# Performance work log

Measured on AMD Instinct MI355X. Metric: run time of the kernel, lower is better.

The kernel has to match this reference:

```python
import jax, jax.numpy as jnp
import numpy as np

MAX_LEN, BATCH, EMB = 512, 32, 41
HID, UNITS = 800, 20
BOND_LENS = jnp.array([1.329, 1.459, 1.525], jnp.float32)
BOND_ANGLES = jnp.array([2.034, 2.119, 1.937], jnp.float32)
INIT_ABC = jnp.array([[0.0, 0.0, 1.0], [0.0, 1.0, 0.0], [1.0, 0.0, 0.0]], jnp.float32)


def _lstm_dir(x, w_ih, w_hh, b, reverse):
    # x: [T, B, in]; returns hidden states [T, B, H]
    T, B, _ = x.shape
    H = w_hh.shape[1]
    xs = jnp.flip(x, 0) if reverse else x
    xw = jnp.einsum('tbi,gi->tbg', xs, w_ih) + b  # precompute input projection

    def step(carry, xt):
        h, c = carry
        gates = xt + h @ w_hh.T
        i, f, g, o = jnp.split(gates, 4, axis=-1)
        c = jax.nn.sigmoid(f) * c + jax.nn.sigmoid(i) * jnp.tanh(g)
        h = jax.nn.sigmoid(o) * jnp.tanh(c)
        return (h, c), h

    init = (jnp.zeros((B, H), x.dtype), jnp.zeros((B, H), x.dtype))
    _, hs = jax.lax.scan(step, init, xw)
    return jnp.flip(hs, 0) if reverse else hs


def _bilstm_layer(x, w_ih, w_hh, b):
    # w_ih: [2, 4H, in]; w_hh: [2, 4H, H]; b: [2, 4H]
    fwd = _lstm_dir(x, w_ih[0], w_hh[0], b[0], False)
    bwd = _lstm_dir(x, w_ih[1], w_hh[1], b[1], True)
    return jnp.concatenate([fwd, bwd], axis=-1)


def _geometric_unit(coords3, triplet):
    # coords3: [3, B, 3] last three atoms; triplet: [B, 3] torsion angles
    A, Bc, C = coords3[0], coords3[1], coords3[2]
    new = []
    for i in range(3):
        Tang, R, P = BOND_ANGLES[i], BOND_LENS[i], triplet[:, i]
        D2 = jnp.stack([-R * jnp.cos(Tang) * jnp.ones_like(P),
                        R * jnp.cos(P) * jnp.sin(Tang),
                        R * jnp.sin(P) * jnp.sin(Tang)], axis=1)  # [B,3]
        BC = C - Bc
        bc = BC / jnp.linalg.norm(BC, axis=1, keepdims=True)
        AB = Bc - A
        N = jnp.cross(AB, bc)
        n = N / jnp.linalg.norm(N, axis=1, keepdims=True)
        M = jnp.stack([bc, jnp.cross(n, bc), n], axis=2)  # [B,3,3]
        D = jnp.einsum('bij,bj->bi', M, D2) + C
        A, Bc, C = Bc, C, D
        new.append(D)
    return jnp.stack([A, Bc, C]), jnp.stack(new)  # carry, [3,B,3]


def setup_inputs() -> dict:
    key = jax.random.key(0)
    ks = jax.random.split(key, 10)
    k = 1.0 / np.sqrt(HID)
    u = lambda kk, shp, lim: jax.random.uniform(kk, shp, jnp.float32, -lim, lim)
    in0, in1 = EMB + 1, 2 * HID
    return {
        'sequences': jax.random.normal(ks[0], (MAX_LEN, BATCH, EMB), jnp.float32),
        'lengths': jnp.full((BATCH,), MAX_LEN, jnp.int64 if jax.config.jax_enable_x64 else jnp.int32),
        'w_ih0': u(ks[1], (2, 4 * HID, in0), k),
        'w_hh0': u(ks[2], (2, 4 * HID, HID), k),
        'b0': u(ks[3], (2, 4 * HID), k),
        'w_ih1': u(ks[4], (2, 4 * HID, in1), k),
        'w_hh1': u(ks[5], (2, 4 * HID, HID), k),
        'b1': u(ks[6], (2, 4 * HID), k),
        'lin_w': u(ks[7], (UNITS, 2 * HID), 1.0 / np.sqrt(2 * HID)),
        'lin_b': u(ks[8], (UNITS,), 1.0 / np.sqrt(2 * HID)),
        'alphabet': jax.random.uniform(ks[9], (UNITS, 3), jnp.float32, -3.14, 3.14),
    }


def reference(sequences, lengths, w_ih0, w_hh0, b0, w_ih1, w_hh1, b1, lin_w, lin_b, alphabet):
    T, B, _ = sequences.shape
    abs_pos = jnp.broadcast_to(jnp.arange(T, dtype=sequences.dtype)[:, None, None], (T, B, 1))
    x = jnp.concatenate([sequences, abs_pos], axis=2)  # [T, B, EMB+1]
    # 2-layer bidirectional LSTM (all lengths == max_len -> packing is identity)
    h = _bilstm_layer(x, w_ih0, w_hh0, b0)
    h = _bilstm_layer(h, w_ih1, w_hh1, b1)  # [T, B, 2H]
    # linear -> softmax over alphabet, trig angle decode
    soft = jax.nn.softmax(h @ lin_w.T + lin_b, axis=2)  # [T, B, UNITS]
    sine = soft @ jnp.sin(alphabet)   # [T, B, 3]
    cosine = soft @ jnp.cos(alphabet)
    out = jnp.arctan2(sine, cosine)   # torsion angle triplets
    # sequential geometric coordinate recurrence over timesteps 1..T-1
    init = jnp.broadcast_to(INIT_ABC[:, None, :], (3, B, 3))
    _, new_coords = jax.lax.scan(_geometric_unit, init, out[1:])  # [T-1, 3, B, 3]
    pred_coords = jnp.concatenate([init, new_coords.reshape(-1, B, 3)], axis=0)
    return pred_coords  # [3 + 3*(T-1), B, 3]
```

## Files before the change

kernel.cpp:

```cpp
#include <hip/hip_runtime.h>
#include <math.h>

#define T_LEN 512
#define NB    32
#define EMB_  41
#define IN0_  42
#define HID_  800
#define G4_   3200
#define IN1_  1600
#define NU    20
#define NCH   100
#define NREP  8

typedef unsigned short u16;
typedef unsigned int   u32;
typedef unsigned long long u64;
typedef __attribute__((ext_vector_type(8))) short short8;
typedef __attribute__((ext_vector_type(4))) float f32x4;

__device__ __forceinline__ float bf2f(u16 v) {
    union { u32 u; float f; } c; c.u = ((u32)v) << 16; return c.f;
}
__device__ __forceinline__ u16 f2bf(float f) {
    union { float f; u32 u; } c; c.f = f;
    u32 r = (c.u + 0x7fffu + ((c.u >> 16) & 1u)) >> 16;
    return (u16)r;
}
__device__ __forceinline__ short cvt_hl(float v, int hl) {
    u16 hi = f2bf(v);
    return hl ? (short)f2bf(v - bf2f(hi)) : (short)hi;
}
__device__ __forceinline__ f32x4 mfma16(short8 a, short8 b, f32x4 c) {
    return __builtin_amdgcn_mfma_f32_16x16x32_bf16(a, b, c, 0, 0, 0);
}
__device__ __forceinline__ u64 aload(const u64* p) {
    return __hip_atomic_load(p, __ATOMIC_RELAXED, __HIP_MEMORY_SCOPE_AGENT);
}
__device__ __forceinline__ void astore(u64* p, u64 v) {
    __hip_atomic_store(p, v, __ATOMIC_RELAXED, __HIP_MEMORY_SCOPE_AGENT);
}
__device__ __forceinline__ int afload(const int* p) {
    return __hip_atomic_load(p, __ATOMIC_RELAXED, __HIP_MEMORY_SCOPE_AGENT);
}
__device__ __forceinline__ void afstore(int* p, int v) {
    __hip_atomic_store(p, v, __ATOMIC_RELAXED, __HIP_MEMORY_SCOPE_AGENT);
}

__global__ __launch_bounds__(256, 1)
void lstm0_persist(const float* __restrict__ seq, const float* __restrict__ wih0,
                   const float* __restrict__ whh0, const float* __restrict__ bias,
                   u16* __restrict__ h0f, u16* __restrict__ hB, int* __restrict__ flags)
{
    __shared__ __align__(16) float part[2048];
    __shared__ __align__(16) u16 stageB[25600];
    __shared__ __align__(16) float w0l[32*48];
    __shared__ __align__(16) float xsl[32*48];
    __shared__ u16 hpk[NB*8];
    const int tid = threadIdx.x;
    const int d = blockIdx.x / NCH, ch = blockIdx.x % NCH;
    const int w = tid >> 6, l = tid & 63;
    const int p = w & 1, hl = w >> 1;
    int* myflags = flags + d*NCH*16;

    short8 wreg[25];
    {
        const int m = l & 15, g = p*2 + (m>>3), j = ch*8 + (m&7);
        const float* base = whh0 + ((size_t)(d*G4_ + g*HID_ + j))*HID_ + (l>>4)*8;
#pragma unroll
        for (int kc = 0; kc < 25; ++kc) {
            float4 f0 = *(const float4*)(base + kc*32);
            float4 f1 = *(const float4*)(base + kc*32 + 4);
            short8 v;
            v[0]=cvt_hl(f0.x,hl); v[1]=cvt_hl(f0.y,hl); v[2]=cvt_hl(f0.z,hl); v[3]=cvt_hl(f0.w,hl);
            v[4]=cvt_hl(f1.x,hl); v[5]=cvt_hl(f1.y,hl); v[6]=cvt_hl(f1.z,hl); v[7]=cvt_hl(f1.w,hl);
            wreg[kc] = v;
        }
    }
    for (int idx = tid; idx < 32*EMB_; idx += 256) {
        int r = idx / EMB_, k = idx % EMB_;
        int ju_ = r >> 2, g = r & 3;
        w0l[r*48 + k] = wih0[((size_t)(d*G4_ + g*HID_ + ch*8 + ju_))*IN0_ + k];
    }
    const int ju = tid >> 5, b = tid & 31;
    const int j = ch*8 + ju;
    const int nt = b >> 4, n = b & 15;
    float biasr[4], wpos[4];
#pragma unroll
    for (int g = 0; g < 4; ++g) {
        biasr[g] = bias[d*G4_ + g*HID_ + j];
        wpos[g]  = wih0[((size_t)(d*G4_ + g*HID_ + j))*IN0_ + EMB_];
    }
    float creg = 0.f;
    __syncthreads();

    for (int s = 0; s < T_LEN; ++s) {
        const int t = d ? (T_LEN-1-s) : s;
        const u64* hq64 = (const u64*)(hB + (size_t)((s&1)*2 + d)*25600);
        u64*      hnq  = (u64*)(hB + (size_t)(((s&1)^1)*2 + d)*25600);

        for (int idx = tid; idx < 32*EMB_; idx += 256)
            xsl[(idx/EMB_)*48 + idx%EMB_] = seq[(size_t)t*(NB*EMB_) + idx];

        if (s > 0 && tid < NCH)
            while (afload(myflags + tid*16) < s) __builtin_amdgcn_s_sleep(1);
        __syncthreads();

        {
            u64 tmp[25];
#pragma unroll
            for (int q = 0; q < 25; ++q) tmp[q] = aload(hq64 + tid + q*256);
#pragma unroll
            for (int q = 0; q < 25; ++q) ((u64*)stageB)[tid + q*256] = tmp[q];
        }
        __syncthreads();

        f32x4 acc0 = {0.f,0.f,0.f,0.f}, acc1 = {0.f,0.f,0.f,0.f};
#pragma unroll 5
        for (int kc = 0; kc < 25; ++kc) {
            short8 b0 = *(const short8*)(stageB + kc*1024 + l*8);
            short8 b1 = *(const short8*)(stageB + kc*1024 + 512 + l*8);
            acc0 = mfma16(wreg[kc], b0, acc0);
            acc1 = mfma16(wreg[kc], b1, acc1);
        }
        {
            const int mrow = (l>>4)*4, nn = l & 15;
#pragma unroll
            for (int r = 0; r < 4; ++r) {
                part[(((p*2+hl)*2 + 0)*16 + mrow + r)*16 + nn] = acc0[r];
                part[(((p*2+hl)*2 + 1)*16 + mrow + r)*16 + nn] = acc1[r];
            }
        }
        __syncthreads();

        float dot0 = 0.f, dot1 = 0.f, dot2 = 0.f, dot3 = 0.f;
        {
            const float* wr = &w0l[ju*4*48];
            const float* xr = &xsl[b*48];
#pragma unroll
            for (int k4 = 0; k4 < 40; k4 += 4) {
                float4 xk = *(const float4*)(xr + k4);
                float4 w0 = *(const float4*)(wr + 0*48 + k4);
                float4 w1 = *(const float4*)(wr + 1*48 + k4);
                float4 w2 = *(const float4*)(wr + 2*48 + k4);
                float4 w3 = *(const float4*)(wr + 3*48 + k4);
                dot0 += w0.x*xk.x + w0.y*xk.y + w0.z*xk.z + w0.w*xk.w;
                dot1 += w1.x*xk.x + w1.y*xk.y + w1.z*xk.z + w1.w*xk.w;
                dot2 += w2.x*xk.x + w2.y*xk.y + w2.z*xk.z + w2.w*xk.w;
                dot3 += w3.x*xk.x + w3.y*xk.y + w3.z*xk.z + w3.w*xk.w;
            }
            float xk = xr[40];
            dot0 += wr[0*48+40]*xk; dot1 += wr[1*48+40]*xk;
            dot2 += wr[2*48+40]*xk; dot3 += wr[3*48+40]*xk;
        }
        float v[4] = {dot0, dot1, dot2, dot3};
#pragma unroll
        for (int g = 0; g < 4; ++g) {
            const int pp = g >> 1, m = (g & 1)*8 + ju;
            v[g] += part[(((pp*2+0)*2 + nt)*16 + m)*16 + n]
                  + part[(((pp*2+1)*2 + nt)*16 + m)*16 + n]
                  + biasr[g] + (float)t * wpos[g];
        }
        float ig = 1.f/(1.f + expf(-v[0]));
        float fg = 1.f/(1.f + expf(-v[1]));
        float gg = tanhf(v[2]);
        float og = 1.f/(1.f + expf(-v[3]));
        creg = fg * creg + ig * gg;
        hpk[b*8 + ju] = f2bf(og * tanhf(creg));
        __syncthreads();

        u64 pk = 0; int xoff = 0;
        if (tid < 64) {
            const int bb = tid >> 1, half = tid & 1;
            const u16* hp = &hpk[bb*8 + half*4];
            pk = (u64)hp[0] | ((u64)hp[1]<<16) | ((u64)hp[2]<<32) | ((u64)hp[3]<<48);
            const int ntb = bb >> 4, llb = ((ch&3)<<4) | (bb&15);
            astore(hnq + ((ch>>2)*2 + ntb)*128 + llb*2 + half, pk);
            xoff = ((d*25 + (ch>>2))*2 + ntb)*128 + llb*2 + half;
        }
        __syncthreads();
        if (tid == 0) afstore(myflags + ch*16, s+1);
        if (tid < 64)
            ((u64*)(h0f + (size_t)t*51200))[xoff] = pk;
    }
}

__global__ __launch_bounds__(256, 1)
void lstm1_persist(const float* __restrict__ wih1, const float* __restrict__ whh1,
                   const float* __restrict__ bias, const float* __restrict__ lin_w,
                   const u16* __restrict__ h0f, u16* __restrict__ hB,
                   int* __restrict__ flags, float* __restrict__ logits)
{
    __shared__ __align__(16) u16 wihL[2*50*512];
    __shared__ __align__(16) u16 stageB[25600];
    __shared__ float lwc[8*NU];
    __shared__ float hblk[8*NB];
    __shared__ u16 hpk[NB*8];
    float* part = (float*)stageB;
    const int tid = threadIdx.x;
    const int d = blockIdx.x / NCH, ch = blockIdx.x % NCH;
    const int w = tid >> 6, l = tid & 63;
    const int p = w & 1, hl = w >> 1;
    int* myflags = flags + d*NCH*16;

    short8 wreg[25];
    {
        const int m = l & 15, g = p*2 + (m>>3), j = ch*8 + (m&7);
        const float* base = whh1 + ((size_t)(d*G4_ + g*HID_ + j))*HID_ + (l>>4)*8;
#pragma unroll
        for (int kc = 0; kc < 25; ++kc) {
            float4 f0 = *(const float4*)(base + kc*32);
            float4 f1 = *(const float4*)(base + kc*32 + 4);
            short8 v;
            v[0]=cvt_hl(f0.x,hl); v[1]=cvt_hl(f0.y,hl); v[2]=cvt_hl(f0.z,hl); v[3]=cvt_hl(f0.w,hl);
            v[4]=cvt_hl(f1.x,hl); v[5]=cvt_hl(f1.y,hl); v[6]=cvt_hl(f1.z,hl); v[7]=cvt_hl(f1.w,hl);
            wreg[kc] = v;
        }
    }
    for (int o = tid; o < 6400; o += 256) {
        int pp = o / 3200, r = o % 3200, kc = r >> 6, ll = r & 63;
        int m = ll & 15, g = pp*2 + (m>>3), jj = ch*8 + (m&7);
        const float* base = wih1 + ((size_t)(d*G4_ + g*HID_ + jj))*IN1_ + kc*32 + (ll>>4)*8;
        float4 f0 = *(const float4*)base;
        float4 f1 = *(const float4*)(base + 4);
        short8 v;
        v[0]=(short)f2bf(f0.x); v[1]=(short)f2bf(f0.y); v[2]=(short)f2bf(f0.z); v[3]=(short)f2bf(f0.w);
        v[4]=(short)f2bf(f1.x); v[5]=(short)f2bf(f1.y); v[6]=(short)f2bf(f1.z); v[7]=(short)f2bf(f1.w);
        *(short8*)&wihL[o*8] = v;
    }
    if (tid < 8*NU) {
        int jju = tid / NU, u = tid % NU;
        lwc[tid] = lin_w[(size_t)u*IN1_ + d*HID_ + ch*8 + jju];
    }
    const int ju = tid >> 5, b = tid & 31;
    const int j = ch*8 + ju;
    const int nt = b >> 4, n = b & 15;
    float biasr[4];
#pragma unroll
    for (int g = 0; g < 4; ++g) biasr[g] = bias[d*G4_ + g*HID_ + j];
    float creg = 0.f;
    float* lrep = logits + (size_t)(ch & (NREP-1)) * (T_LEN*NB*NU);
    __syncthreads();

    for (int s = 0; s < T_LEN; ++s) {
        const int t = d ? (T_LEN-1-s) : s;
        const u64* hq64 = (const u64*)(hB + (size_t)((s&1)*2 + d)*25600);
        u64*      hnq  = (u64*)(hB + (size_t)(((s&1)^1)*2 + d)*25600);

        f32x4 acc0 = {0.f,0.f,0.f,0.f}, acc1 = {0.f,0.f,0.f,0.f};
        {
            const u16* xb = h0f + (size_t)t*51200;
#pragma unroll 5
            for (int kc = 0; kc < 25; ++kc) {
                const int idx = hl*25 + kc;
                short8 a  = *(const short8*)&wihL[(p*50 + idx)*512 + l*8];
                short8 b0 = *(const short8*)(xb + idx*1024 + l*8);
                short8 b1 = *(const short8*)(xb + idx*1024 + 512 + l*8);
                acc0 = mfma16(a, b0, acc0);
                acc1 = mfma16(a, b1, acc1);
            }
        }

        if (s > 0 && tid < NCH)
            while (afload(myflags + tid*16) < s) __builtin_amdgcn_s_sleep(1);
        __syncthreads();

        {
            u64 tmp[25];
#pragma unroll
            for (int q = 0; q < 25; ++q) tmp[q] = aload(hq64 + tid + q*256);
#pragma unroll
            for (int q = 0; q < 25; ++q) ((u64*)stageB)[tid + q*256] = tmp[q];
        }
        __syncthreads();

#pragma unroll 5
        for (int kc = 0; kc < 25; ++kc) {
            short8 b0 = *(const short8*)(stageB + kc*1024 + l*8);
            short8 b1 = *(const short8*)(stageB + kc*1024 + 512 + l*8);
            acc0 = mfma16(wreg[kc], b0, acc0);
            acc1 = mfma16(wreg[kc], b1, acc1);
        }
        __syncthreads();
        {
            const int mrow = (l>>4)*4, nn = l & 15;
#pragma unroll
            for (int r = 0; r < 4; ++r) {
                part[(((p*2+hl)*2 + 0)*16 + mrow + r)*16 + nn] = acc0[r];
                part[(((p*2+hl)*2 + 1)*16 + mrow + r)*16 + nn] = acc1[r];
            }
        }
        __syncthreads();

        float v[4];
#pragma unroll
        for (int g = 0; g < 4; ++g) {
            const int pp = g >> 1, m = (g & 1)*8 + ju;
            v[g] = part[(((pp*2+0)*2 + nt)*16 + m)*16 + n]
                 + part[(((pp*2+1)*2 + nt)*16 + m)*16 + n] + biasr[g];
        }
        float ig = 1.f/(1.f + expf(-v[0]));
        float fg = 1.f/(1.f + expf(-v[1]));
        float gg = tanhf(v[2]);
        float og = 1.f/(1.f + expf(-v[3]));
        creg = fg * creg + ig * gg;
        float hn = og * tanhf(creg);
        hblk[ju*NB + b] = hn;
        hpk[b*8 + ju] = f2bf(hn);
        __syncthreads();

        if (tid < 64) {
            const int bb = tid >> 1, half = tid & 1;
            const u16* hp = &hpk[bb*8 + half*4];
            u64 pk = (u64)hp[0] | ((u64)hp[1]<<16) | ((u64)hp[2]<<32) | ((u64)hp[3]<<48);
            const int ntb = bb >> 4, llb = ((ch&3)<<4) | (bb&15);
            astore(hnq + ((ch>>2)*2 + ntb)*128 + llb*2 + half, pk);
        }
        __syncthreads();
        if (tid == 0) afstore(myflags + ch*16, s+1);

        {
            float* lg = lrep + (size_t)t*(NB*NU);
            for (int q = tid; q < NB*NU; q += 256) {
                int kk = q + (ch & 31)*NU;
                if (kk >= NB*NU) kk -= NB*NU;
                const int bb = kk / NU, uu = kk % NU;
                float sum = 0.f;
#pragma unroll
                for (int qq = 0; qq < 8; ++qq) sum += lwc[qq*NU + uu] * hblk[qq*NB + bb];
                atomicAdd(lg + kk, sum);
            }
        }
    }
}

__global__ __launch_bounds__(256)
void epilogue(const float* __restrict__ logits, const float* __restrict__ lin_b,
              const float* __restrict__ alphabet, float* __restrict__ cs)
{
    __shared__ float sa[NU*3], ca[NU*3], lb[NU];
    const int tid = threadIdx.x;
    if (tid < NU*3) { float al = alphabet[tid]; sa[tid] = sinf(al); ca[tid] = cosf(al); }
    if (tid < NU) lb[tid] = lin_b[tid];
    __syncthreads();
    const int row = blockIdx.x*256 + tid;
    if (row >= T_LEN*NB) return;
    float lg[NU];
#pragma unroll 4
    for (int u = 0; u < NU; ++u) lg[u] = lb[u];
    for (int r = 0; r < NREP; ++r) {
        const float* lp = logits + (size_t)r*(T_LEN*NB*NU) + (size_t)row*NU;
#pragma unroll 4
        for (int u = 0; u < NU; ++u) lg[u] += lp[u];
    }
    float m = -1e30f;
#pragma unroll 4
    for (int u = 0; u < NU; ++u) m = fmaxf(m, lg[u]);
    float ssum = 0.f;
#pragma unroll 4
    for (int u = 0; u < NU; ++u) { lg[u] = expf(lg[u] - m); ssum += lg[u]; }
    float inv = 1.f / ssum;
#pragma unroll
    for (int i = 0; i < 3; ++i) {
        float sv = 0.f, cv = 0.f;
#pragma unroll 4
        for (int u = 0; u < NU; ++u) {
            float sw = lg[u] * inv;
            sv += sw * sa[u*3 + i];
            cv += sw * ca[u*3 + i];
        }
        float rinv = rsqrtf(fmaxf(sv*sv + cv*cv, 1e-30f));
        *(float2*)(cs + ((size_t)row*3 + i)*2) = make_float2(cv*rinv, sv*rinv);
    }
}

__global__ __launch_bounds__(64)
void geometry(const float* __restrict__ cs, float* __restrict__ out)
{
    const int b = threadIdx.x;
    if (b >= NB) return;
    const float blen[3] = {1.329f, 1.459f, 1.525f};
    const float bang[3] = {2.034f, 2.119f, 1.937f};
    float sT[3], cT[3];
#pragma unroll
    for (int i = 0; i < 3; ++i) { sT[i] = sinf(bang[i]); cT[i] = cosf(bang[i]); }

    float Ax=0.f,Ay=0.f,Az=1.f, Bx=0.f,By=1.f,Bz=0.f, Cx=1.f,Cy=0.f,Cz=0.f;
    out[(0*NB + b)*3 + 0] = 0.f; out[(0*NB + b)*3 + 1] = 0.f; out[(0*NB + b)*3 + 2] = 1.f;
    out[(1*NB + b)*3 + 0] = 0.f; out[(1*NB + b)*3 + 1] = 1.f; out[(1*NB + b)*3 + 2] = 0.f;
    out[(2*NB + b)*3 + 0] = 1.f; out[(2*NB + b)*3 + 1] = 0.f; out[(2*NB + b)*3 + 2] = 0.f;

    for (int t = 1; t < T_LEN; ++t) {
        float2 pc[3];
#pragma unroll
        for (int i = 0; i < 3; ++i)
            pc[i] = *(const float2*)(cs + (((size_t)t*NB + b)*3 + i)*2);
#pragma unroll
        for (int i = 0; i < 3; ++i) {
            float R = blen[i];
            float d2x = -R*cT[i], d2y = R*pc[i].x*sT[i], d2z = R*pc[i].y*sT[i];
            float bcx = Cx-Bx, bcy = Cy-By, bcz = Cz-Bz;
            float inv = rsqrtf(bcx*bcx + bcy*bcy + bcz*bcz);
            bcx *= inv; bcy *= inv; bcz *= inv;
            float abx = Bx-Ax, aby = By-Ay, abz = Bz-Az;
            float nx = aby*bcz - abz*bcy;
            float ny = abz*bcx - abx*bcz;
            float nz = abx*bcy - aby*bcx;
            inv = rsqrtf(fmaxf(nx*nx + ny*ny + nz*nz, 1e-30f));
            nx *= inv; ny *= inv; nz *= inv;
            float mx = ny*bcz - nz*bcy;
            float my = nz*bcx - nx*bcz;
            float mz = nx*bcy - ny*bcx;
            float Dx = bcx*d2x + mx*d2y + nx*d2z + Cx;
            float Dy = bcy*d2x + my*d2y + ny*d2z + Cy;
            float Dz = bcz*d2x + mz*d2y + nz*d2z + Cz;
            Ax=Bx; Ay=By; Az=Bz; Bx=Cx; By=Cy; Bz=Cz; Cx=Dx; Cy=Dy; Cz=Dz;
            const int r = 3 + (t-1)*3 + i;
            out[((size_t)r*NB + b)*3 + 0] = Dx;
            out[((size_t)r*NB + b)*3 + 1] = Dy;
            out[((size_t)r*NB + b)*3 + 2] = Dz;
        }
    }
}

extern "C" void kernel_launch(void* const* d_in, const int* in_sizes, int n_in,
                              void* d_out, int out_size, void* d_ws, size_t ws_size,
                              hipStream_t stream)
{
    (void)in_sizes; (void)n_in; (void)out_size; (void)ws_size;
    const float* seq   = (const float*)d_in[0];
    const float* w_ih0 = (const float*)d_in[2];
    const float* w_hh0 = (const float*)d_in[3];
    const float* b0    = (const float*)d_in[4];
    const float* w_ih1 = (const float*)d_in[5];
    const float* w_hh1 = (const float*)d_in[6];
    const float* b1    = (const float*)d_in[7];
    const float* lin_w = (const float*)d_in[8];
    const float* lin_b = (const float*)d_in[9];
    const float* alpha = (const float*)d_in[10];

    char* ws = (char*)d_ws;
    size_t off = 0;
    u16* h0f   = (u16*)(ws + off); off += 52428800ull;
    u16* hB    = (u16*)(ws + off); off += 204800ull;
    int* flagsL0 = (int*)(ws + off); off += 12800ull;
    int* flagsL1 = (int*)(ws + off); off += 12800ull;
    float* logits = (float*)(ws + off); off += (size_t)NREP*1310720ull;
    float* cs = (float*)(ws + off); off += 393216ull;

    hipMemsetAsync(hB, 0, 204800 + 12800 + 12800, stream);
    hipMemsetAsync(logits, 0, (size_t)NREP*1310720ull, stream);

    lstm0_persist<<<dim3(2*NCH), dim3(256), 0, stream>>>(seq, w_ih0, w_hh0, b0, h0f, hB, flagsL0);

    hipMemsetAsync(hB, 0, 204800, stream);
    lstm1_persist<<<dim3(2*NCH), dim3(256), 0, stream>>>(w_ih1, w_hh1, b1, lin_w, h0f, hB,
                                                         flagsL1, logits);

    epilogue<<<dim3(64), dim3(256), 0, stream>>>(logits, lin_b, alpha, cs);
    geometry<<<dim3(1), dim3(64), 0, stream>>>(cs, (float*)d_out);
}
```

Measured before the change: 9.664 ms.

## Halve layer-0 blocks, fold input projection into MFMA, compute logits from staged h

Layer 0 now runs on 50 blocks per direction instead of 100. Each wave holds both the hi and lo bf16 weight halves for one gate, so the split-precision work moves into extra MFMAs rather than being spread across waves. The input projection is done with MFMA on bf16 hi/lo split inputs instead of scalar FP32 dot products. Layer 1 drops the replicated atomicAdd logit accumulation and instead computes each direction's logits directly from the full hidden state already staged in LDS, one step late, with a final tail step. This cuts the number of blocks polled per step and removes the atomics and the 8-way replica reduction, at the cost of more MFMA work per block and a redundant logit computation spread across blocks.

```diff
diff --git a/kernel.cpp b/kernel.cpp
--- a/kernel.cpp
+++ b/kernel.cpp
@@ -9,8 +9,8 @@
 #define G4_   3200
 #define IN1_  1600
 #define NU    20
-#define NCH   100
-#define NREP  8
+#define NCH0  50
+#define NCH1  100
 
 typedef unsigned short u16;
 typedef unsigned int   u32;
@@ -53,44 +53,61 @@
 {
     __shared__ __align__(16) float part[2048];
     __shared__ __align__(16) u16 stageB[25600];
-    __shared__ __align__(16) float w0l[32*48];
-    __shared__ __align__(16) float xsl[32*48];
-    __shared__ u16 hpk[NB*8];
+    __shared__ __align__(16) u16 xf[2][2048];
+    __shared__ u16 hpk[NB*16];
     const int tid = threadIdx.x;
-    const int d = blockIdx.x / NCH, ch = blockIdx.x % NCH;
+    const int d = blockIdx.x / NCH0, ch = blockIdx.x % NCH0;
     const int w = tid >> 6, l = tid & 63;
-    const int p = w & 1, hl = w >> 1;
-    int* myflags = flags + d*NCH*16;
-
-    short8 wreg[25];
+    int* myflags = flags + d*NCH0*16;
+
+    short8 wreg[2][25];
     {
-        const int m = l & 15, g = p*2 + (m>>3), j = ch*8 + (m&7);
-        const float* base = whh0 + ((size_t)(d*G4_ + g*HID_ + j))*HID_ + (l>>4)*8;
+        const int m = l & 15, j = ch*16 + m;
+        const float* base = whh0 + ((size_t)(d*G4_ + w*HID_ + j))*HID_ + (l>>4)*8;
 #pragma unroll
         for (int kc = 0; kc < 25; ++kc) {
             float4 f0 = *(const float4*)(base + kc*32);
             float4 f1 = *(const float4*)(base + kc*32 + 4);
-            short8 v;
-            v[0]=cvt_hl(f0.x,hl); v[1]=cvt_hl(f0.y,hl); v[2]=cvt_hl(f0.z,hl); v[3]=cvt_hl(f0.w,hl);
-            v[4]=cvt_hl(f1.x,hl); v[5]=cvt_hl(f1.y,hl); v[6]=cvt_hl(f1.z,hl); v[7]=cvt_hl(f1.w,hl);
-            wreg[kc] = v;
-        }
-    }
-    for (int idx = tid; idx < 32*EMB_; idx += 256) {
-        int r = idx / EMB_, k = idx % EMB_;
-        int ju_ = r >> 2, g = r & 3;
-        w0l[r*48 + k] = wih0[((size_t)(d*G4_ + g*HID_ + ch*8 + ju_))*IN0_ + k];
-    }
-    const int ju = tid >> 5, b = tid & 31;
-    const int j = ch*8 + ju;
+            float vv[8] = {f0.x,f0.y,f0.z,f0.w,f1.x,f1.y,f1.z,f1.w};
+            short8 vh, vl;
+#pragma unroll
+            for (int e = 0; e < 8; ++e) {
+                u16 hi = f2bf(vv[e]);
+                vh[e] = (short)hi;
+                vl[e] = (short)f2bf(vv[e] - bf2f(hi));
+            }
+            wreg[0][kc] = vh; wreg[1][kc] = vl;
+        }
+    }
+    short8 wx[2][2];
+    {
+        const int m = l & 15, j = ch*16 + m;
+#pragma unroll
+        for (int kc2 = 0; kc2 < 2; ++kc2) {
+            short8 vh, vl;
+#pragma unroll
+            for (int e = 0; e < 8; ++e) {
+                int k = kc2*32 + (l>>4)*8 + e;
+                float v = (k < EMB_) ? wih0[((size_t)(d*G4_ + w*HID_ + j))*IN0_ + k] : 0.f;
+                u16 hi = f2bf(v);
+                vh[e] = (short)hi;
+                vl[e] = (short)f2bf(v - bf2f(hi));
+            }
+            wx[0][kc2] = vh; wx[1][kc2] = vl;
+        }
+    }
+    const int jub = tid >> 5, b = tid & 31;
     const int nt = b >> 4, n = b & 15;
-    float biasr[4], wpos[4];
-#pragma unroll
-    for (int g = 0; g < 4; ++g) {
-        biasr[g] = bias[d*G4_ + g*HID_ + j];
-        wpos[g]  = wih0[((size_t)(d*G4_ + g*HID_ + j))*IN0_ + EMB_];
-    }
-    float creg = 0.f;
+    float biasr[2][4], wpos[2][4], creg[2] = {0.f, 0.f};
+#pragma unroll
+    for (int pi = 0; pi < 2; ++pi) {
+        const int j = ch*16 + jub + pi*8;
+#pragma unroll
+        for (int g = 0; g < 4; ++g) {
+            biasr[pi][g] = bias[d*G4_ + g*HID_ + j];
+            wpos[pi][g]  = wih0[((size_t)(d*G4_ + g*HID_ + j))*IN0_ + EMB_];
+        }
+    }
     __syncthreads();
 
     for (int s = 0; s < T_LEN; ++s) {
@@ -98,10 +115,21 @@
         const u64* hq64 = (const u64*)(hB + (size_t)((s&1)*2 + d)*25600);
         u64*      hnq  = (u64*)(hB + (size_t)(((s&1)^1)*2 + d)*25600);
 
-        for (int idx = tid; idx < 32*EMB_; idx += 256)
-            xsl[(idx/EMB_)*48 + idx%EMB_] = seq[(size_t)t*(NB*EMB_) + idx];
-
-        if (s > 0 && tid < NCH)
+        {
+            const int e0 = tid*8;
+            const int kc2 = e0 >> 10, nt_ = (e0 >> 9) & 1, l_ = (e0 >> 3) & 63;
+            const int kb = kc2*32 + (l_>>4)*8;
+            const float* sp = seq + (size_t)t*(NB*EMB_) + (nt_*16 + (l_&15))*EMB_;
+#pragma unroll
+            for (int e = 0; e < 8; ++e) {
+                int k = kb + e;
+                float v = (k < EMB_) ? sp[k] : 0.f;
+                u16 hi = f2bf(v);
+                xf[0][e0+e] = hi;
+                xf[1][e0+e] = f2bf(v - bf2f(hi));
+            }
+        }
+        if (s > 0 && tid < NCH0)
             while (afload(myflags + tid*16) < s) __builtin_amdgcn_s_sleep(1);
         __syncthreads();
 
@@ -119,69 +147,92 @@
         for (int kc = 0; kc < 25; ++kc) {
             short8 b0 = *(const short8*)(stageB + kc*1024 + l*8);
             short8 b1 = *(const short8*)(stageB + kc*1024 + 512 + l*8);
-            acc0 = mfma16(wreg[kc], b0, acc0);
-            acc1 = mfma16(wreg[kc], b1, acc1);
+            acc0 = mfma16(wreg[0][kc], b0, acc0);
+            acc0 = mfma16(wreg[1][kc], b0, acc0);
+            acc1 = mfma16(wreg[0][kc], b1, acc1);
+            acc1 = mfma16(wreg[1][kc], b1, acc1);
+        }
+#pragma unroll
+        for (int kc2 = 0; kc2 < 2; ++kc2) {
+            short8 xh0 = *(const short8*)(&xf[0][(kc2*2+0)*512] + l*8);
+            short8 xl0 = *(const short8*)(&xf[1][(kc2*2+0)*512] + l*8);
+            short8 xh1 = *(const short8*)(&xf[0][(kc2*2+1)*512] + l*8);
+            short8 xl1 = *(const short8*)(&xf[1][(kc2*2+1)*512] + l*8);
+            acc0 = mfma16(wx[0][kc2], xh0, acc0);
+            acc0 = mfma16(wx[0][kc2], xl0, acc0);
+            acc0 = mfma16(wx[1][kc2], xh0, acc0);
+            acc1 = mfma16(wx[0][kc2], xh1, acc1);
+            acc1 = mfma16(wx[0][kc2], xl1, acc1);
+            acc1 = mfma16(wx[1][kc2], xh1, acc1);
         }
         {
             const int mrow = (l>>4)*4, nn = l & 15;
 #pragma unroll
             for (int r = 0; r < 4; ++r) {
-                part[(((p*2+hl)*2 + 0)*16 + mrow + r)*16 + nn] = acc0[r];
-                part[(((p*2+hl)*2 + 1)*16 + mrow + r)*16 + nn] = acc1[r];
+                part[((w*2 + 0)*16 + mrow + r)*16 + nn] = acc0[r];
+                part[((w*2 + 1)*16 + mrow + r)*16 + nn] = acc1[r];
             }
         }
         __syncthreads();
 
-        float dot0 = 0.f, dot1 = 0.f, dot2 = 0.f, dot3 = 0.f;
-        {
-            const float* wr = &w0l[ju*4*48];
-            const float* xr = &xsl[b*48];
-#pragma unroll
-            for (int k4 = 0; k4 < 40; k4 += 4) {
-                float4 xk = *(const float4*)(xr + k4);
-                float4 w0 = *(const float4*)(wr + 0*48 + k4);
-                float4 w1 = *(const float4*)(wr + 1*48 + k4);
-                float4 w2 = *(const float4*)(wr + 2*48 + k4);
-                float4 w3 = *(const float4*)(wr + 3*48 + k4);
-                dot0 += w0.x*xk.x + w0.y*xk.y + w0.z*xk.z + w0.w*xk.w;
-                dot1 += w1.x*xk.x + w1.y*xk.y + w1.z*xk.z + w1.w*xk.w;
-                dot2 += w2.x*xk.x + w2.y*xk.y + w2.z*xk.z + w2.w*xk.w;
-                dot3 += w3.x*xk.x + w3.y*xk.y + w3.z*xk.z + w3.w*xk.w;
-            }
-            float xk = xr[40];
-            dot0 += wr[0*48+40]*xk; dot1 += wr[1*48+40]*xk;
-            dot2 += wr[2*48+40]*xk; dot3 += wr[3*48+40]*xk;
-        }
-        float v[4] = {dot0, dot1, dot2, dot3};
-#pragma unroll
-        for (int g = 0; g < 4; ++g) {
-            const int pp = g >> 1, m = (g & 1)*8 + ju;
-            v[g] += part[(((pp*2+0)*2 + nt)*16 + m)*16 + n]
-                  + part[(((pp*2+1)*2 + nt)*16 + m)*16 + n]
-                  + biasr[g] + (float)t * wpos[g];
-        }
-        float ig = 1.f/(1.f + expf(-v[0]));
-        float fg = 1.f/(1.f + expf(-v[1]));
-        float gg = tanhf(v[2]);
-        float og = 1.f/(1.f + expf(-v[3]));
-        creg = fg * creg + ig * gg;
-        hpk[b*8 + ju] = f2bf(og * tanhf(creg));
+#pragma unroll
+        for (int pi = 0; pi < 2; ++pi) {
+            const int ju = jub + pi*8;
+            float v[4];
+#pragma unroll
+            for (int g = 0; g < 4; ++g)
+                v[g] = part[((g*2 + nt)*16 + ju)*16 + n] + biasr[pi][g] + (float)t * wpos[pi][g];
+            float ig = 1.f/(1.f + expf(-v[0]));
+            float fg = 1.f/(1.f + expf(-v[1]));
+            float gg = tanhf(v[2]);
+            float og = 1.f/(1.f + expf(-v[3]));
+            creg[pi] = fg * creg[pi] + ig * gg;
+            hpk[b*16 + ju] = f2bf(og * tanhf(creg[pi]));
+        }
         __syncthreads();
 
         u64 pk = 0; int xoff = 0;
-        if (tid < 64) {
-            const int bb = tid >> 1, half = tid & 1;
-            const u16* hp = &hpk[bb*8 + half*4];
+        if (tid < 128) {
+            const int half = tid & 1;
+            const int pn   = (tid >> 1) & 15;
+            const int ng   = (tid >> 5) & 1;
+            const int pnt  = (tid >> 6) & 1;
+            const int bb   = pnt*16 + pn;
+            const int jbase = ng*8 + half*4;
+            const u16* hp = &hpk[bb*16 + jbase];
             pk = (u64)hp[0] | ((u64)hp[1]<<16) | ((u64)hp[2]<<32) | ((u64)hp[3]<<48);
-            const int ntb = bb >> 4, llb = ((ch&3)<<4) | (bb&15);
-            astore(hnq + ((ch>>2)*2 + ntb)*128 + llb*2 + half, pk);
-            xoff = ((d*25 + (ch>>2))*2 + ntb)*128 + llb*2 + half;
+            const int lst = (((ch&1)*2 + ng) << 4) | pn;
+            const int kc  = ch >> 1;
+            astore(hnq + (kc*2 + pnt)*128 + lst*2 + half, pk);
+            xoff = ((d*25 + kc)*2 + pnt)*128 + lst*2 + half;
         }
         __syncthreads();
         if (tid == 0) afstore(myflags + ch*16, s+1);
-        if (tid < 64)
+        if (tid < 128)
             ((u64*)(h0f + (size_t)t*51200))[xoff] = pk;
     }
+}
+
+__device__ __forceinline__ void logit_from_stage(const u16* __restrict__ stageB,
+        const float* __restrict__ lin_w, float* __restrict__ logits,
+        int d, int ch, int tprev, int tid)
+{
+    const int ol = tid >> 5, ln = tid & 31;
+    if (ol >= 7) return;
+    const int o = ch*7 + ol;
+    if (o >= NB*NU) return;
+    const int bb = o / NU, uu = o % NU;
+    const int nt_ = bb >> 4, bn = bb & 15;
+    const float* wrow = lin_w + (size_t)uu*IN1_ + d*HID_;
+    float sum = 0.f;
+    for (int k = ln*25; k < ln*25 + 25; ++k) {
+        const int kc = k >> 5, w5 = k & 31;
+        const int l_ = ((w5>>3)<<4) | bn, i_ = w5 & 7;
+        sum += bf2f(stageB[kc*1024 + nt_*512 + l_*8 + i_]) * wrow[k];
+    }
+#pragma unroll
+    for (int off2 = 16; off2; off2 >>= 1) sum += __shfl_down(sum, off2, 32);
+    if (ln == 0) logits[((size_t)d*T_LEN + tprev)*640 + o] = sum;
 }
 
 __global__ __launch_bounds__(256, 1)
@@ -192,15 +243,13 @@
 {
     __shared__ __align__(16) u16 wihL[2*50*512];
     __shared__ __align__(16) u16 stageB[25600];
-    __shared__ float lwc[8*NU];
-    __shared__ float hblk[8*NB];
+    __shared__ __align__(16) float part[2048];
     __shared__ u16 hpk[NB*8];
-    float* part = (float*)stageB;
     const int tid = threadIdx.x;
-    const int d = blockIdx.x / NCH, ch = blockIdx.x % NCH;
+    const int d = blockIdx.x / NCH1, ch = blockIdx.x % NCH1;
     const int w = tid >> 6, l = tid & 63;
     const int p = w & 1, hl = w >> 1;
-    int* myflags = flags + d*NCH*16;
+    int* myflags = flags + d*NCH1*16;
 
     short8 wreg[25];
     {
@@ -227,10 +276,6 @@
         v[4]=(short)f2bf(f1.x); v[5]=(short)f2bf(f1.y); v[6]=(short)f2bf(f1.z); v[7]=(short)f2bf(f1.w);
         *(short8*)&wihL[o*8] = v;
     }
-    if (tid < 8*NU) {
-        int jju = tid / NU, u = tid % NU;
-        lwc[tid] = lin_w[(size_t)u*IN1_ + d*HID_ + ch*8 + jju];
-    }
     const int ju = tid >> 5, b = tid & 31;
     const int j = ch*8 + ju;
     const int nt = b >> 4, n = b & 15;
@@ -238,7 +283,6 @@
 #pragma unroll
     for (int g = 0; g < 4; ++g) biasr[g] = bias[d*G4_ + g*HID_ + j];
     float creg = 0.f;
-    float* lrep = logits + (size_t)(ch & (NREP-1)) * (T_LEN*NB*NU);
     __syncthreads();
 
     for (int s = 0; s < T_LEN; ++s) {
@@ -260,7 +304,7 @@
             }
         }
 
-        if (s > 0 && tid < NCH)
+        if (s > 0 && tid < NCH1)
             while (afload(myflags + tid*16) < s) __builtin_amdgcn_s_sleep(1);
         __syncthreads();
 
@@ -280,7 +324,6 @@
             acc0 = mfma16(wreg[kc], b0, acc0);
             acc1 = mfma16(wreg[kc], b1, acc1);
         }
-        __syncthreads();
         {
             const int mrow = (l>>4)*4, nn = l & 15;
 #pragma unroll
@@ -304,7 +347,6 @@
         float og = 1.f/(1.f + expf(-v[3]));
         creg = fg * creg + ig * gg;
         float hn = og * tanhf(creg);
-        hblk[ju*NB + b] = hn;
         hpk[b*8 + ju] = f2bf(hn);
         __syncthreads();
 
@@ -318,19 +360,23 @@
         __syncthreads();
         if (tid == 0) afstore(myflags + ch*16, s+1);
 
-        {
-            float* lg = lrep + (size_t)t*(NB*NU);
-            for (int q = tid; q < NB*NU; q += 256) {
-                int kk = q + (ch & 31)*NU;
-                if (kk >= NB*NU) kk -= NB*NU;
-                const int bb = kk / NU, uu = kk % NU;
-                float sum = 0.f;
-#pragma unroll
-                for (int qq = 0; qq < 8; ++qq) sum += lwc[qq*NU + uu] * hblk[qq*NB + bb];
-                atomicAdd(lg + kk, sum);
-            }
-        }
-    }
+        if (s > 0)
+            logit_from_stage(stageB, lin_w, logits, d, ch,
+                             d ? (T_LEN - s) : (s - 1), tid);
+    }
+    if (tid < NCH1)
+        while (afload(myflags + tid*16) < T_LEN) __builtin_amdgcn_s_sleep(1);
+    __syncthreads();
+    {
+        const u64* hq64 = (const u64*)(hB + (size_t)((T_LEN&1)*2 + d)*25600);
+        u64 tmp[25];
+#pragma unroll
+        for (int q = 0; q < 25; ++q) tmp[q] = aload(hq64 + tid + q*256);
+#pragma unroll
+        for (int q = 0; q < 25; ++q) ((u64*)stageB)[tid + q*256] = tmp[q];
+    }
+    __syncthreads();
+    logit_from_stage(stageB, lin_w, logits, d, ch, d ? 0 : (T_LEN - 1), tid);
 }
 
 __global__ __launch_bounds__(256)
@@ -344,17 +390,15 @@
     __syncthreads();
     const int row = blockIdx.x*256 + tid;
     if (row >= T_LEN*NB) return;
+    const int t = row >> 5, b = row & 31;
     float lg[NU];
-#pragma unroll 4
-    for (int u = 0; u < NU; ++u) lg[u] = lb[u];
-    for (int r = 0; r < NREP; ++r) {
-        const float* lp = logits + (size_t)r*(T_LEN*NB*NU) + (size_t)row*NU;
-#pragma unroll 4
-        for (int u = 0; u < NU; ++u) lg[u] += lp[u];
-    }
     float m = -1e30f;
 #pragma unroll 4
-    for (int u = 0; u < NU; ++u) m = fmaxf(m, lg[u]);
+    for (int u = 0; u < NU; ++u) {
+        lg[u] = lb[u] + logits[(size_t)t*640 + b*NU + u]
+                      + logits[((size_t)T_LEN + t)*640 + b*NU + u];
+        m = fmaxf(m, lg[u]);
+    }
     float ssum = 0.f;
 #pragma unroll 4
     for (int u = 0; u < NU; ++u) { lg[u] = expf(lg[u] - m); ssum += lg[u]; }
@@ -442,19 +486,18 @@
     size_t off = 0;
     u16* h0f   = (u16*)(ws + off); off += 52428800ull;
     u16* hB    = (u16*)(ws + off); off += 204800ull;
-    int* flagsL0 = (int*)(ws + off); off += 12800ull;
+    int* flagsL0 = (int*)(ws + off); off += 6400ull;
     int* flagsL1 = (int*)(ws + off); off += 12800ull;
-    float* logits = (float*)(ws + off); off += (size_t)NREP*1310720ull;
+    float* logits = (float*)(ws + off); off += 2621440ull;
     float* cs = (float*)(ws + off); off += 393216ull;
 
-    hipMemsetAsync(hB, 0, 204800 + 12800 + 12800, stream);
-    hipMemsetAsync(logits, 0, (size_t)NREP*1310720ull, stream);
-
-    lstm0_persist<<<dim3(2*NCH), dim3(256), 0, stream>>>(seq, w_ih0, w_hh0, b0, h0f, hB, flagsL0);
+    hipMemsetAsync(hB, 0, 204800 + 6400 + 12800, stream);
+
+    lstm0_persist<<<dim3(2*NCH0), dim3(256), 0, stream>>>(seq, w_ih0, w_hh0, b0, h0f, hB, flagsL0);
 
     hipMemsetAsync(hB, 0, 204800, stream);
-    lstm1_persist<<<dim3(2*NCH), dim3(256), 0, stream>>>(w_ih1, w_hh1, b1, lin_w, h0f, hB,
-                                                         flagsL1, logits);
+    lstm1_persist<<<dim3(2*NCH1), dim3(256), 0, stream>>>(w_ih1, w_hh1, b1, lin_w, h0f, hB,
+                                                          flagsL1, logits);
 
     epilogue<<<dim3(64), dim3(256), 0, stream>>>(logits, lin_b, alpha, cs);
     geometry<<<dim3(1), dim3(64), 0, stream>>>(cs, (float*)d_out);
```

Result: slower. 10.47 ms (+8.3%).

## Compute output logits from staged full hidden state instead of per-chunk atomics

Applied to the files above, without the earlier changes.

Rather than having each chunk block atomically accumulate its 8-unit partial contribution to the logits across replicated buffers, each block now owns a few (batch, unit) output entries. It computes them fully from the previous step's complete hidden state, which is already staged in shared memory, using register-resident lin_w rows and a warp reduction. This removes the per-step atomics, the replicated logits buffers and their memset, and the replica reduction in the epilogue. It also drops one barrier by giving the partial-sum scratch its own shared buffer. The cost is extra registers, plus a final wait on all flags and a reload of the last hidden state after the loop.

```diff
diff --git a/kernel.cpp b/kernel.cpp
--- a/kernel.cpp
+++ b/kernel.cpp
@@ -10,7 +10,6 @@
 #define IN1_  1600
 #define NU    20
 #define NCH   100
-#define NREP  8
 
 typedef unsigned short u16;
 typedef unsigned int   u32;
@@ -192,10 +191,8 @@
 {
     __shared__ __align__(16) u16 wihL[2*50*512];
     __shared__ __align__(16) u16 stageB[25600];
-    __shared__ float lwc[8*NU];
-    __shared__ float hblk[8*NB];
+    __shared__ __align__(16) float part[2048];
     __shared__ u16 hpk[NB*8];
-    float* part = (float*)stageB;
     const int tid = threadIdx.x;
     const int d = blockIdx.x / NCH, ch = blockIdx.x % NCH;
     const int w = tid >> 6, l = tid & 63;
@@ -227,9 +224,17 @@
         v[4]=(short)f2bf(f1.x); v[5]=(short)f2bf(f1.y); v[6]=(short)f2bf(f1.z); v[7]=(short)f2bf(f1.w);
         *(short8*)&wihL[o*8] = v;
     }
-    if (tid < 8*NU) {
-        int jju = tid / NU, u = tid % NU;
-        lwc[tid] = lin_w[(size_t)u*IN1_ + d*HID_ + ch*8 + jju];
+    const int ol = tid >> 5, ln = tid & 31;
+    const int lo = ch*7 + ol;
+    const bool lown = (ol < 7) && (lo < NB*NU);
+    int lofs = 0;
+    float wlin[25];
+    if (lown) {
+        const int bb = lo / NU, uu = lo % NU;
+        lofs = (bb >> 4)*512 + ((((ln >> 3) << 4) | (bb & 15)))*8 + (ln & 7);
+        const float* wrow = lin_w + (size_t)uu*IN1_ + d*HID_ + ln;
+#pragma unroll
+        for (int i = 0; i < 25; ++i) wlin[i] = wrow[i*32];
     }
     const int ju = tid >> 5, b = tid & 31;
     const int j = ch*8 + ju;
@@ -238,7 +243,6 @@
 #pragma unroll
     for (int g = 0; g < 4; ++g) biasr[g] = bias[d*G4_ + g*HID_ + j];
     float creg = 0.f;
-    float* lrep = logits + (size_t)(ch & (NREP-1)) * (T_LEN*NB*NU);
     __syncthreads();
 
     for (int s = 0; s < T_LEN; ++s) {
@@ -280,7 +284,6 @@
             acc0 = mfma16(wreg[kc], b0, acc0);
             acc1 = mfma16(wreg[kc], b1, acc1);
         }
-        __syncthreads();
         {
             const int mrow = (l>>4)*4, nn = l & 15;
 #pragma unroll
@@ -304,7 +307,6 @@
         float og = 1.f/(1.f + expf(-v[3]));
         creg = fg * creg + ig * gg;
         float hn = og * tanhf(creg);
-        hblk[ju*NB + b] = hn;
         hpk[b*8 + ju] = f2bf(hn);
         __syncthreads();
 
@@ -318,17 +320,41 @@
         __syncthreads();
         if (tid == 0) afstore(myflags + ch*16, s+1);
 
-        {
-            float* lg = lrep + (size_t)t*(NB*NU);
-            for (int q = tid; q < NB*NU; q += 256) {
-                int kk = q + (ch & 31)*NU;
-                if (kk >= NB*NU) kk -= NB*NU;
-                const int bb = kk / NU, uu = kk % NU;
-                float sum = 0.f;
-#pragma unroll
-                for (int qq = 0; qq < 8; ++qq) sum += lwc[qq*NU + uu] * hblk[qq*NB + bb];
-                atomicAdd(lg + kk, sum);
+        if (s > 0 && lown) {
+            float sum = 0.f;
+#pragma unroll
+            for (int i = 0; i < 25; ++i)
+                sum += bf2f(stageB[i*1024 + lofs]) * wlin[i];
+#pragma unroll
+            for (int off2 = 16; off2; off2 >>= 1) sum += __shfl_down(sum, off2, 32);
+            if (ln == 0) {
+                const int tprev = d ? (T_LEN - s) : (s - 1);
+                logits[((size_t)d*T_LEN + tprev)*640 + lo] = sum;
             }
+        }
+    }
+    if (tid < NCH)
+        while (afload(myflags + tid*16) < T_LEN) __builtin_amdgcn_s_sleep(1);
+    __syncthreads();
+    {
+        const u64* hq64 = (const u64*)(hB + (size_t)((T_LEN&1)*2 + d)*25600);
+        u64 tmp[25];
+#pragma unroll
+        for (int q = 0; q < 25; ++q) tmp[q] = aload(hq64 + tid + q*256);
+#pragma unroll
+        for (int q = 0; q < 25; ++q) ((u64*)stageB)[tid + q*256] = tmp[q];
+    }
+    __syncthreads();
+    if (lown) {
+        float sum = 0.f;
+#pragma unroll
+        for (int i = 0; i < 25; ++i)
+            sum += bf2f(stageB[i*1024 + lofs]) * wlin[i];
+#pragma unroll
+        for (int off2 = 16; off2; off2 >>= 1) sum += __shfl_down(sum, off2, 32);
+        if (ln == 0) {
+            const int tprev = d ? 0 : (T_LEN - 1);
+            logits[((size_t)d*T_LEN + tprev)*640 + lo] = sum;
         }
     }
 }
@@ -344,17 +370,15 @@
     __syncthreads();
     const int row = blockIdx.x*256 + tid;
     if (row >= T_LEN*NB) return;
+    const int t = row >> 5, b = row & 31;
     float lg[NU];
-#pragma unroll 4
-    for (int u = 0; u < NU; ++u) lg[u] = lb[u];
-    for (int r = 0; r < NREP; ++r) {
-        const float* lp = logits + (size_t)r*(T_LEN*NB*NU) + (size_t)row*NU;
-#pragma unroll 4
-        for (int u = 0; u < NU; ++u) lg[u] += lp[u];
-    }
     float m = -1e30f;
 #pragma unroll 4
-    for (int u = 0; u < NU; ++u) m = fmaxf(m, lg[u]);
+    for (int u = 0; u < NU; ++u) {
+        lg[u] = lb[u] + logits[(size_t)t*640 + b*NU + u]
+                      + logits[((size_t)T_LEN + t)*640 + b*NU + u];
+        m = fmaxf(m, lg[u]);
+    }
     float ssum = 0.f;
 #pragma unroll 4
     for (int u = 0; u < NU; ++u) { lg[u] = expf(lg[u] - m); ssum += lg[u]; }
@@ -444,11 +468,10 @@
     u16* hB    = (u16*)(ws + off); off += 204800ull;
     int* flagsL0 = (int*)(ws + off); off += 12800ull;
     int* flagsL1 = (int*)(ws + off); off += 12800ull;
-    float* logits = (float*)(ws + off); off += (size_t)NREP*1310720ull;
+    float* logits = (float*)(ws + off); off += 2621440ull;
     float* cs = (float*)(ws + off); off += 393216ull;
 
     hipMemsetAsync(hB, 0, 204800 + 12800 + 12800, stream);
-    hipMemsetAsync(logits, 0, (size_t)NREP*1310720ull, stream);
 
     lstm0_persist<<<dim3(2*NCH), dim3(256), 0, stream>>>(seq, w_ih0, w_hh0, b0, h0f, hB, flagsL0);
 
```

Result: faster. 9.444 ms (-2.3%).
